# Kernel tuning notes

Hardware: AMD Instinct MI355X
Metric: run time of the kernel (lower is better)

## Reference

```python
import jax, jax.numpy as jnp
import numpy as np

B, N, F, G, H = 8, 1024, 512, 128, 8
D = F // H  # head_dim = 64


def setup_inputs() -> dict:
    key = jax.random.key(0)
    ks = jax.random.split(key, 24)
    def lin(k, fan_in, shape):
        return jax.random.normal(k, shape, jnp.float32) / np.sqrt(fan_in)
    return {
        "features": jax.random.normal(ks[0], (B, N, F), jnp.float32),
        "geometry": jax.random.normal(ks[1], (B, N, G), jnp.float32),
        "coords": jax.random.normal(ks[2], (B, N, 3), jnp.float32),
        # nnx.MultiHeadAttention params (q/k/v/out dense, with bias)
        "wq": lin(ks[3], F, (F, F)), "bq": jnp.zeros((F,), jnp.float32),
        "wk": lin(ks[4], F, (F, F)), "bk": jnp.zeros((F,), jnp.float32),
        "wv": lin(ks[5], F, (F, F)), "bv": jnp.zeros((F,), jnp.float32),
        "wo": lin(ks[6], F, (F, F)), "bo": jnp.zeros((F,), jnp.float32),
        # geometry q/k/v linears
        "gq_w": lin(ks[7], G, (G, F)), "gq_b": jnp.zeros((F,), jnp.float32),
        "gk_w": lin(ks[8], G, (G, F)), "gk_b": jnp.zeros((F,), jnp.float32),
        "gv_w": lin(ks[9], G, (G, F)), "gv_b": jnp.zeros((F,), jnp.float32),
        # distance MLP: Linear(1->H), gelu, Linear(H->H)
        "d1_w": lin(ks[10], 1, (1, H)), "d1_b": jnp.zeros((H,), jnp.float32),
        "d2_w": lin(ks[11], H, (H, H)), "d2_b": jnp.zeros((H,), jnp.float32),
        # output projection
        "op_w": lin(ks[12], F, (F, F)), "op_b": jnp.zeros((F,), jnp.float32),
    }


def _forward(features, geometry, coords,
             wq, bq, wk, bk, wv, bv, wo, bo,
             gq_w, gq_b, gk_w, gk_b, gv_w, gv_b,
             d1_w, d1_b, d2_w, d2_b, op_w, op_b):
    scale = jnp.sqrt(jnp.float32(D))
    # --- standard multi-head self-attention branch (nnx.MultiHeadAttention) ---
    q = (features @ wq + bq).reshape(B, N, H, D)
    k = (features @ wk + bk).reshape(B, N, H, D)
    v = (features @ wv + bv).reshape(B, N, H, D)
    scores = jnp.einsum("bqhd,bkhd->bhqk", q, k) / scale
    attn = jax.nn.softmax(scores, axis=-1)
    feat_att = jnp.einsum("bhqk,bkhd->bqhd", attn, v).reshape(B, N, F)
    feat_att = feat_att @ wo + bo
    # --- geometry attention branch ---
    gq = geometry @ gq_w + gq_b
    gk = geometry @ gk_w + gk_b
    gv = geometry @ gv_w + gv_b
    g_scores = jnp.einsum("bqd,bkd->bqk", gq, gk) / scale
    # pairwise distances (B,N,N,1); clamp for sqrt-at-zero safety (diagonal)
    diff = coords[:, :, None, :] - coords[:, None, :, :]
    dist = jnp.sqrt(jnp.maximum(jnp.sum(diff * diff, -1, keepdims=True), 1e-12))
    dw = jax.nn.gelu(dist @ d1_w + d1_b) @ d2_w + d2_b  # (B,N,N,H)
    # transpose to (B,H,N,N) then mean over heads == mean over last axis
    g_scores = g_scores + jnp.mean(dw, axis=-1)
    g_attn = jax.nn.softmax(g_scores, axis=-1)
    geom_att = jnp.einsum("bqk,bkd->bqd", g_attn, gv)
    return (feat_att + geom_att) @ op_w + op_b


def reference(features, geometry, coords,
              wq, bq, wk, bk, wv, bv, wo, bo,
              gq_w, gq_b, gk_w, gk_b, gv_w, gv_b,
              d1_w, d1_b, d2_w, d2_b, op_w, op_b):
    return _forward(features, geometry, coords,
                    wq, bq, wk, bk, wv, bv, wo, bo,
                    gq_w, gq_b, gk_w, gk_b, gv_w, gv_b,
                    d1_w, d1_b, d2_w, d2_b, op_w, op_b)
```

## Files before the change

### kernel.cpp

```cpp
#include <hip/hip_runtime.h>

typedef __bf16 bf16_t;
typedef __bf16 bf16x8 __attribute__((ext_vector_type(8)));
typedef __bf16 bf16x4v __attribute__((ext_vector_type(4)));
typedef float f32x4 __attribute__((ext_vector_type(4)));

#define MFMA16(a, b, c) __builtin_amdgcn_mfma_f32_16x16x32_bf16((a), (b), (c), 0, 0, 0)

static constexpr int B_ = 8, N_ = 1024, F_ = 512, H_ = 8;
static constexpr int M_ = B_ * N_;
static constexpr float LOG2E = 1.4426950408889634f;

__device__ __forceinline__ void gl_lds16(const bf16_t* gsrc, bf16_t* ldst) {
  __builtin_amdgcn_global_load_lds(
      (const __attribute__((address_space(1))) void*)gsrc,
      (__attribute__((address_space(3))) void*)ldst, 16, 0, 0);
}

__device__ __forceinline__ float gelu_tanh(float u) {
  float g = 0.7978845608028654f * fmaf(0.044715f * u * u, u, u);
  float e = __expf(2.f * g);
  float t = 1.f - 2.f / (e + 1.f);
  return 0.5f * u * (1.f + t);
}

struct PrepArgs {
  const float *features, *geometry;
  const float *wq, *wk, *wv, *wo, *op_w;
  const float *gq_w, *gk_w, *gv_w;
  const float *bq, *bk, *bv, *gq_b, *gv_b;
  const float *d1w, *d1b, *d2w, *d2b;
  bf16_t *featBF, *geomBF, *WqkvT, *GqvT2, *WoT, *OpT;
  float *bqkv, *gqvb2, *dlut;
};

static constexpr int PR_C0 = 4096;
static constexpr int PR_C1 = PR_C0 + 1024;
static constexpr int PR_WQ = PR_C1 + 256;
static constexpr int PR_WK = PR_WQ + 256;
static constexpr int PR_WV = PR_WK + 256;
static constexpr int PR_WO = PR_WV + 256;
static constexpr int PR_OP = PR_WO + 256;
static constexpr int PR_GVT = PR_OP + 64;
static constexpr int PR_WEFF = PR_GVT + 4;
static constexpr int PR_BEFF = PR_WEFF + 1;
static constexpr int PR_B1 = PR_BEFF + 6;
static constexpr int PR_B2 = PR_B1 + 2;
static constexpr int PR_LUT = PR_B2 + 16;
static constexpr int PR_TOTAL = PR_LUT;

__device__ __forceinline__ void prep_cast(const float* __restrict__ in,
                                          bf16_t* __restrict__ out, int blk) {
  int i = blk * 256 + threadIdx.x;
  float4 v = ((const float4*)in)[i];
  bf16x4v o;
  o[0] = (bf16_t)v.x; o[1] = (bf16_t)v.y; o[2] = (bf16_t)v.z; o[3] = (bf16_t)v.w;
  ((bf16x4v*)out)[i] = o;
}

__device__ __forceinline__ void prep_transpose(const float* __restrict__ W,
                                               bf16_t* __restrict__ Wt,
                                               int K, int N, int ldo, int idx,
                                               float (*t)[33]) {
  const int bx = idx & 15, by = idx >> 4;
  const int kb = by * 32, cb = bx * 32;
  const int tx = threadIdx.x & 31, ty = threadIdx.x >> 5;
#pragma unroll
  for (int i = 0; i < 4; ++i)
    t[ty * 4 + i][tx] = W[(long)(kb + ty * 4 + i) * N + cb + tx];
  __syncthreads();
#pragma unroll
  for (int i = 0; i < 4; ++i)
    Wt[(long)(cb + ty * 4 + i) * ldo + kb + tx] = (bf16_t)t[tx][ty * 4 + i];
}

__device__ __forceinline__ bf16x8 cvt2x4(float4 a, float4 b) {
  bf16x8 v;
  v[0] = (bf16_t)a.x; v[1] = (bf16_t)a.y; v[2] = (bf16_t)a.z; v[3] = (bf16_t)a.w;
  v[4] = (bf16_t)b.x; v[5] = (bf16_t)b.y; v[6] = (bf16_t)b.z; v[7] = (bf16_t)b.w;
  return v;
}

__global__ __launch_bounds__(256) void k_prep(PrepArgs p) {
  __shared__ alignas(16) char psh[16384];
  float (*tsh)[33] = (float (*)[33])psh;
  const int blk = blockIdx.x;
  if (blk < PR_C0) {
    prep_cast(p.features, p.featBF, blk);
  } else if (blk < PR_C1) {
    prep_cast(p.geometry, p.geomBF, blk - PR_C0);
  } else if (blk < PR_WQ) {
    prep_transpose(p.wq, p.WqkvT, 512, 512, 512, blk - PR_C1, tsh);
  } else if (blk < PR_WK) {
    prep_transpose(p.wk, p.WqkvT + 512 * 512, 512, 512, 512, blk - PR_WQ, tsh);
  } else if (blk < PR_WV) {
    prep_transpose(p.wv, p.WqkvT + 1024 * 512, 512, 512, 512, blk - PR_WK, tsh);
  } else if (blk < PR_WO) {
    prep_transpose(p.wo, p.WoT, 512, 512, 512, blk - PR_WV, tsh);
  } else if (blk < PR_OP) {
    prep_transpose(p.op_w, p.OpT, 512, 512, 512, blk - PR_WO, tsh);
  } else if (blk < PR_GVT) {
    prep_transpose(p.gv_w, p.GqvT2 + 128 * 128, 128, 512, 128, blk - PR_OP, tsh);
  } else if (blk < PR_WEFF) {
    bf16_t (*As)[64] = (bf16_t (*)[64])psh;
    bf16_t (*Bs)[64] = (bf16_t (*)[64])(psh + 8192);
    const int wb = blk - PR_GVT;
    const int gBrow = (wb >> 1) * 64;
    const int hBcol = (wb & 1) * 64;
    const int tid = threadIdx.x;
    const int w4 = tid >> 6, lane = tid & 63;
    const int lr = lane & 15, lg = lane >> 4;
    const int wr = w4 >> 1, wc = w4 & 1;
    const int srow = tid >> 2, scol = (tid & 3) << 4;
    f32x4 zero = {0.f, 0.f, 0.f, 0.f};
    f32x4 acc[2][2] = {{zero, zero}, {zero, zero}};
    for (int f0 = 0; f0 < 512; f0 += 64) {
#pragma unroll
      for (int hh = 0; hh < 2; ++hh) {
        const long offA = (long)(gBrow + srow) * 512 + f0 + scol + hh * 8;
        float4 a0 = *(const float4*)(p.gk_w + offA);
        float4 a1 = *(const float4*)(p.gk_w + offA + 4);
        *(bf16x8*)(&As[srow][scol + hh * 8]) = cvt2x4(a0, a1);
        const long offB = (long)(hBcol + srow) * 512 + f0 + scol + hh * 8;
        float4 b0 = *(const float4*)(p.gq_w + offB);
        float4 b1 = *(const float4*)(p.gq_w + offB + 4);
        *(bf16x8*)(&Bs[srow][scol + hh * 8]) = cvt2x4(b0, b1);
      }
      __syncthreads();
#pragma unroll
      for (int ks = 0; ks < 2; ++ks) {
        bf16x8 a[2], b[2];
#pragma unroll
        for (int i = 0; i < 2; ++i) {
          a[i] = *(const bf16x8*)(&As[wr * 32 + i * 16 + lr][ks * 32 + lg * 8]);
          b[i] = *(const bf16x8*)(&Bs[wc * 32 + i * 16 + lr][ks * 32 + lg * 8]);
        }
#pragma unroll
        for (int mf = 0; mf < 2; ++mf)
#pragma unroll
          for (int nf = 0; nf < 2; ++nf)
            acc[mf][nf] = MFMA16(a[mf], b[nf], acc[mf][nf]);
      }
      __syncthreads();
    }
#pragma unroll
    for (int mf = 0; mf < 2; ++mf)
#pragma unroll
      for (int nf = 0; nf < 2; ++nf)
#pragma unroll
        for (int rg = 0; rg < 4; ++rg) {
          const int row = gBrow + wr * 32 + mf * 16 + lg * 4 + rg;
          const int col = hBcol + wc * 32 + nf * 16 + lr;
          p.GqvT2[(long)row * 128 + col] = (bf16_t)acc[mf][nf][rg];
        }
  } else if (blk < PR_BEFF) {
    const int g = threadIdx.x;
    if (g < 128) {
      float s = 0.f;
      for (int f = 0; f < 512; ++f) s = fmaf(p.gq_b[f], p.gk_w[(long)g * 512 + f], s);
      p.gqvb2[g] = s;
    }
  } else if (blk < PR_B1) {
    int i = (blk - PR_BEFF) * 256 + threadIdx.x;
    p.bqkv[i] = i < 512 ? p.bq[i] : (i < 1024 ? p.bk[i - 512] : p.bv[i - 1024]);
  } else if (blk < PR_B2) {
    int i = (blk - PR_B1) * 256 + threadIdx.x;
    p.gqvb2[128 + i] = p.gv_b[i];
  } else {
    int i = (blk - PR_B2) * 256 + threadIdx.x;
    float d = (i + 0.5f) * (16.f / 4096.f);
    float s = 0.f;
#pragma unroll
    for (int h = 0; h < 8; ++h) s += p.d2b[h];
    s *= 0.125f;
#pragma unroll
    for (int j = 0; j < 8; ++j) {
      float w2 = 0.f;
#pragma unroll
      for (int h = 0; h < 8; ++h) w2 += p.d2w[j * 8 + h];
      s = fmaf(gelu_tanh(fmaf(d, p.d1w[j], p.d1b[j])), w2 * 0.125f, s);
    }
    p.dlut[i] = s;
  }
}

struct GemmArgs {
  const bf16_t* A; const bf16_t* Bt;
  const float* bias; const float* addSrc; const bf16_t* addSrcB;
  const float* coords; const float* lut;
  float* outF; bf16_t* outB;
  bf16_t* outT;
  int vtileFrom;
  long strideAb; long strideBb;
  int lda, ldb, K, ldout;
  float scale;
};

__device__ __forceinline__ void gemm128_core(const GemmArgs& g, int mBase, int cBase,
                                             bf16_t (*As)[64], bf16_t (*Bs)[64]) {
  const int tid = threadIdx.x;
  const int w = tid >> 6, lane = tid & 63;
  const int lr = lane & 15, lg = lane >> 4;
  const int wr = w >> 1, wc = w & 1;
  const int batch = mBase >> 10;

  const int srow = lane >> 3;
  const int scol = (lane & 7) * 8;
  const bf16_t* Ag = g.A + (long)batch * g.strideAb +
                     (long)((mBase & 1023) + w * 32 + srow) * g.lda + scol;
  const bf16_t* Bg = g.Bt + (long)batch * g.strideBb +
                     (long)(cBase + w * 32 + srow) * g.ldb + scol;
  bf16_t* Al = &As[w * 32][0];
  bf16_t* Bl = &Bs[w * 32][0];

  f32x4 zero = {0.f, 0.f, 0.f, 0.f};
  f32x4 acc[4][4];
#pragma unroll
  for (int i = 0; i < 4; ++i)
#pragma unroll
    for (int j = 0; j < 4; ++j) acc[i][j] = zero;

  for (int k0 = 0; k0 < g.K; k0 += 64) {
#pragma unroll
    for (int is = 0; is < 4; ++is) {
      gl_lds16(Ag + (long)(is * 8) * g.lda + k0, Al + is * 8 * 64);
      gl_lds16(Bg + (long)(is * 8) * g.ldb + k0, Bl + is * 8 * 64);
    }
    __syncthreads();
#pragma unroll
    for (int ks = 0; ks < 2; ++ks) {
      bf16x8 a[4], b[4];
#pragma unroll
      for (int i = 0; i < 4; ++i) {
        a[i] = *(const bf16x8*)(&As[wr * 64 + i * 16 + lr][ks * 32 + lg * 8]);
        b[i] = *(const bf16x8*)(&Bs[wc * 64 + i * 16 + lr][ks * 32 + lg * 8]);
      }
#pragma unroll
      for (int mf = 0; mf < 4; ++mf)
#pragma unroll
        for (int nf = 0; nf < 4; ++nf)
          acc[mf][nf] = MFMA16(a[mf], b[nf], acc[mf][nf]);
    }
    __syncthreads();
  }

  const int c0 = cBase + wc * 64;
  float bias4[4];
#pragma unroll
  for (int nf = 0; nf < 4; ++nf)
    bias4[nf] = g.bias ? g.bias[c0 + nf * 16 + lr] : 0.f;
  const bool vtile = (g.outT != nullptr) && (cBase >= g.vtileFrom);
#pragma unroll
  for (int mf = 0; mf < 4; ++mf) {
    const int r0 = mBase + wr * 64 + mf * 16 + lg * 4;
    const int r0b = r0 & 1023;
#pragma unroll
    for (int nf = 0; nf < 4; ++nf) {
      const int c = c0 + nf * 16 + lr;
      if (vtile) {
        bf16x4v vv;
#pragma unroll
        for (int rg = 0; rg < 4; ++rg)
          vv[rg] = (bf16_t)(acc[mf][nf][rg] * g.scale + bias4[nf]);
        *(bf16x4v*)(&g.outT[((long)batch * 512 + (c - g.vtileFrom)) * 1024 + r0b]) = vv;
      } else {
#pragma unroll
        for (int rg = 0; rg < 4; ++rg) {
          const int r = r0 + rg;
          float v = acc[mf][nf][rg] * g.scale + bias4[nf];
          if (g.addSrc) v += g.addSrc[(long)r * g.ldout + c];
          const long oi = (long)r * g.ldout + c;
          if (g.outF) g.outF[oi] = v;
          if (g.outB) g.outB[oi] = (bf16_t)v;
        }
      }
    }
  }
}

__global__ __launch_bounds__(256) void k_gemm128_dual(GemmArgs g1, GemmArgs g2) {
  __shared__ alignas(16) bf16_t As[128][64];
  __shared__ alignas(16) bf16_t Bs[128][64];
  const int bx = blockIdx.x;
  if (bx < 768) {
    gemm128_core(g1, (bx / 12) * 128, (bx % 12) * 128, As, Bs);
  } else {
    const int i = bx - 768;
    gemm128_core(g2, (i / 5) * 128, (i % 5) * 128, As, Bs);
  }
}

__device__ __forceinline__ void gemm128_dist(const GemmArgs& g, int mBase, int cBase,
                                             char* smemc) {
  bf16_t (*As)[64] = (bf16_t (*)[64])smemc;
  bf16_t (*Bs)[64] = (bf16_t (*)[64])(smemc + 16384);
  bf16_t* Lut = (bf16_t*)(smemc + 32768);
  const int tid = threadIdx.x;
  const int w = tid >> 6, lane = tid & 63;
  const int lr = lane & 15, lg = lane >> 4;
  const int wr = w >> 1, wc = w & 1;
  const int batch = mBase >> 10;

  {
    const float4* src = (const float4*)g.lut;
#pragma unroll
    for (int i = 0; i < 4; ++i) {
      float4 v = src[tid + i * 256];
      bf16x4v o;
      o[0] = (bf16_t)(v.x * LOG2E); o[1] = (bf16_t)(v.y * LOG2E);
      o[2] = (bf16_t)(v.z * LOG2E); o[3] = (bf16_t)(v.w * LOG2E);
      ((bf16x4v*)Lut)[tid + i * 256] = o;
    }
  }

  const int srow = lane >> 3;
  const int scol = (lane & 7) * 8;
  const bf16_t* Ag = g.A + (long)batch * g.strideAb +
                     (long)((mBase & 1023) + w * 32 + srow) * g.lda + scol;
  const bf16_t* Bg = g.Bt + (long)batch * g.strideBb +
                     (long)(cBase + w * 32 + srow) * g.ldb + scol;
  bf16_t* Al = &As[w * 32][0];
  bf16_t* Bl = &Bs[w * 32][0];

  f32x4 zero = {0.f, 0.f, 0.f, 0.f};
  f32x4 acc[4][4];
#pragma unroll
  for (int i = 0; i < 4; ++i)
#pragma unroll
    for (int j = 0; j < 4; ++j) acc[i][j] = zero;

  for (int k0 = 0; k0 < g.K; k0 += 64) {
#pragma unroll
    for (int is = 0; is < 4; ++is) {
      gl_lds16(Ag + (long)(is * 8) * g.lda + k0, Al + is * 8 * 64);
      gl_lds16(Bg + (long)(is * 8) * g.ldb + k0, Bl + is * 8 * 64);
    }
    __syncthreads();
#pragma unroll
    for (int ks = 0; ks < 2; ++ks) {
      bf16x8 a[4], b[4];
#pragma unroll
      for (int i = 0; i < 4; ++i) {
        a[i] = *(const bf16x8*)(&As[wr * 64 + i * 16 + lr][ks * 32 + lg * 8]);
        b[i] = *(const bf16x8*)(&Bs[wc * 64 + i * 16 + lr][ks * 32 + lg * 8]);
      }
#pragma unroll
      for (int mf = 0; mf < 4; ++mf)
#pragma unroll
        for (int nf = 0; nf < 4; ++nf)
          acc[mf][nf] = MFMA16(a[mf], b[nf], acc[mf][nf]);
    }
    __syncthreads();
  }

  const int c0 = cBase + wc * 64;
  float ckx[4], cky[4], ckz[4];
#pragma unroll
  for (int nf = 0; nf < 4; ++nf) {
    const float* ck = g.coords + ((long)batch * 1024 + c0 + nf * 16 + lr) * 3;
    ckx[nf] = ck[0]; cky[nf] = ck[1]; ckz[nf] = ck[2];
  }
#pragma unroll
  for (int mf = 0; mf < 4; ++mf) {
    const int r0 = mBase + wr * 64 + mf * 16 + lg * 4;
    float cqx[4], cqy[4], cqz[4];
#pragma unroll
    for (int rg = 0; rg < 4; ++rg) {
      const float* cq = g.coords + ((long)batch * 1024 + ((r0 + rg) & 1023)) * 3;
      cqx[rg] = cq[0]; cqy[rg] = cq[1]; cqz[rg] = cq[2];
    }
#pragma unroll
    for (int nf = 0; nf < 4; ++nf) {
      const int c = c0 + nf * 16 + lr;
#pragma unroll
      for (int rg = 0; rg < 4; ++rg) {
        const int r = r0 + rg;
        float v = acc[mf][nf][rg] * g.scale;
        float dx = cqx[rg] - ckx[nf], dy = cqy[rg] - cky[nf], dz = cqz[rg] - ckz[nf];
        float d = sqrtf(fmaxf(dx * dx + dy * dy + dz * dz, 1e-12f));
        int idx = (int)(d * 256.f);
        idx = idx > 4095 ? 4095 : idx;
        g.outB[(long)r * g.ldout + c] = (bf16_t)exp2f(v + (float)Lut[idx]);
      }
    }
  }
}

__device__ __forceinline__ void flash_core(const bf16_t* __restrict__ QKV,
                                           const bf16_t* __restrict__ Vt,
                                           bf16_t* __restrict__ fatt,
                                           int qx, int bh, char* smemc) {
  bf16_t (*Ks)[64][64] = (bf16_t (*)[64][64])smemc;
  bf16_t (*Vs)[64][64] = (bf16_t (*)[64][64])(smemc + 16384);
  char* Plb = smemc + 32768;
  const int wave = threadIdx.x >> 6, lane = threadIdx.x & 63;
  const int lr = lane & 15, lg = (lane >> 4) & 3;
  const int b = bh >> 3, h = bh & 7;
  const int qbase = qx * 128 + wave * 32;

  const bf16_t* Qb = QKV + (long)b * 1024 * 1536 + h * 64;
  const bf16_t* Kb = Qb + 512;
  const bf16_t* Vg = Vt + ((long)b * 512 + h * 64) * 1024;

  constexpr float SCL = 0.18033688011112042f;
  bf16x8 q_[2][2];
#pragma unroll
  for (int qf = 0; qf < 2; ++qf)
#pragma unroll
    for (int dh = 0; dh < 2; ++dh) {
      bf16x8 raw = *(const bf16x8*)(Qb + (long)(qbase + qf * 16 + lr) * 1536 +
                                    dh * 32 + lg * 8);
#pragma unroll
      for (int j = 0; j < 8; ++j) q_[qf][dh][j] = (bf16_t)((float)raw[j] * SCL);
    }
  bf16x8 onesb;
#pragma unroll
  for (int j = 0; j < 8; ++j) onesb[j] = (bf16_t)1.0f;

  const int srow = lane >> 3;
  const int scol = (((lane & 7) ^ srow) << 3);
  const bf16_t* KgB = Kb + (long)(wave * 16 + srow) * 1536 + scol;
  const bf16_t* VgB = Vg + (long)(wave * 16 + srow) * 1024 + scol;

  auto stage = [&](int buf, int kt) {
#pragma unroll
    for (int i = 0; i < 2; ++i) {
      gl_lds16(KgB + (long)(kt + i * 8) * 1536, &Ks[buf][wave * 16 + i * 8][0]);
      gl_lds16(VgB + (long)(i * 8) * 1024 + kt, &Vs[buf][wave * 16 + i * 8][0]);
    }
  };

  f32x4 zero = {0.f, 0.f, 0.f, 0.f};
  f32x4 oacc[2][4] = {{zero, zero, zero, zero}, {zero, zero, zero, zero}};
  f32x4 oL[2] = {zero, zero};
  const int swz = (lr & 7) << 4;
  const int swp = (lr & 6) << 3;
  char* PlW = Plb + wave * 2048;

  stage(0, 0);
  asm volatile("s_waitcnt vmcnt(0)" ::: "memory");
  __syncthreads();

  auto tile = [&](const int buf, int t) __attribute__((always_inline)) {
    if (t < 15) stage(buf ^ 1, (t + 1) * 64);
    const char* KB = (const char*)&Ks[buf][0][0];
    const char* VB = (const char*)&Vs[buf][0][0];
#pragma unroll
    for (int kk = 0; kk < 2; ++kk) {
      f32x4 S[2][2];
      __builtin_amdgcn_s_setprio(1);
#pragma unroll
      for (int kh = 0; kh < 2; ++kh) {
        const int row = kk * 32 + kh * 16 + lr;
        bf16x8 k0 = *(const bf16x8*)(KB + row * 128 + ((lg * 16) ^ swz));
        bf16x8 k1 = *(const bf16x8*)(KB + row * 128 + ((64 + lg * 16) ^ swz));
#pragma unroll
        for (int qf = 0; qf < 2; ++qf) {
          f32x4 tt = MFMA16(k0, q_[qf][0], zero);
          S[qf][kh] = MFMA16(k1, q_[qf][1], tt);
        }
      }
      __builtin_amdgcn_s_setprio(0);
#pragma unroll
      for (int qf = 0; qf < 2; ++qf)
#pragma unroll
        for (int kh = 0; kh < 2; ++kh) {
          bf16x4v pp;
#pragma unroll
          for (int r = 0; r < 4; ++r) pp[r] = (bf16_t)exp2f(S[qf][kh][r]);
          *(bf16x4v*)(PlW + qf * 1024 + lr * 64 + ((kh * 32 + lg * 8) ^ swp)) = pp;
        }
      asm volatile("s_waitcnt lgkmcnt(0)" ::: "memory");
      const bf16x8 pa0 = *(const bf16x8*)(PlW + lr * 64 + ((lg * 16) ^ swp));
      const bf16x8 pa1 = *(const bf16x8*)(PlW + 1024 + lr * 64 + ((lg * 16) ^ swp));
      __builtin_amdgcn_s_setprio(1);
#pragma unroll
      for (int ct = 0; ct < 4; ++ct) {
        const int vrow = ct * 16 + lr;
        bf16x8 vf = *(const bf16x8*)(VB + vrow * 128 + ((kk * 64 + lg * 16) ^ swz));
        oacc[0][ct] = MFMA16(pa0, vf, oacc[0][ct]);
        oacc[1][ct] = MFMA16(pa1, vf, oacc[1][ct]);
      }
      oL[0] = MFMA16(pa0, onesb, oL[0]);
      oL[1] = MFMA16(pa1, onesb, oL[1]);
      __builtin_amdgcn_s_setprio(0);
    }
    asm volatile("s_waitcnt vmcnt(0)" ::: "memory");
    __syncthreads();
  };

  for (int tt = 0; tt < 8; ++tt) {
    tile(0, tt * 2);
    tile(1, tt * 2 + 1);
  }

#pragma unroll
  for (int qf = 0; qf < 2; ++qf)
#pragma unroll
    for (int r = 0; r < 4; ++r) {
      float inv = 1.f / oL[qf][r];
      int q = qbase + qf * 16 + lg * 4 + r;
      bf16_t* orow = fatt + ((long)b * 1024 + q) * 512 + h * 64;
#pragma unroll
      for (int ct = 0; ct < 4; ++ct)
        orow[ct * 16 + lr] = (bf16_t)(oacc[qf][ct][r] * inv);
    }
}

__global__ __launch_bounds__(256) void k_gsc_flash(GemmArgs g,
                                                   const bf16_t* __restrict__ QKV,
                                                   const bf16_t* __restrict__ Vt,
                                                   bf16_t* __restrict__ fatt) {
  __shared__ alignas(16) char smem[40960];
  const int bx = blockIdx.x;
  if (bx < 512) {
    gemm128_dist(g, (bx >> 3) * 128, (bx & 7) * 128, smem);
  } else {
    const int fid = bx - 512;
    flash_core(QKV, Vt, fatt, fid & 7, fid >> 3, smem);
  }
}

template <int RSUM>
__device__ __forceinline__ void m64_loop(const GemmArgs& g, int mBase, int cBase,
                                         bf16_t (*As)[64], bf16_t (*Bs)[64],
                                         f32x4 (*acc)[2], f32x4* lacc) {
  const int tid = threadIdx.x;
  const int w = tid >> 6, lane = tid & 63;
  const int lr = lane & 15, lg = lane >> 4;
  const int wr = w >> 1, wc = w & 1;
  const int batch = mBase >> 10;

  const int srow = lane >> 3;
  const int scol = (lane & 7) * 8;
  const bf16_t* Ag = g.A + (long)batch * g.strideAb +
                     (long)((mBase & 1023) + w * 16 + srow) * g.lda + scol;
  const bf16_t* Bg = g.Bt + (long)batch * g.strideBb +
                     (long)(cBase + w * 16 + srow) * g.ldb + scol;
  bf16_t* Al = &As[w * 16][0];
  bf16_t* Bl = &Bs[w * 16][0];

  bf16x8 onesb;
#pragma unroll
  for (int j = 0; j < 8; ++j) onesb[j] = (bf16_t)1.0f;

  for (int k0 = 0; k0 < g.K; k0 += 64) {
#pragma unroll
    for (int is = 0; is < 2; ++is) {
      gl_lds16(Ag + (long)(is * 8) * g.lda + k0, Al + is * 8 * 64);
      gl_lds16(Bg + (long)(is * 8) * g.ldb + k0, Bl + is * 8 * 64);
    }
    __syncthreads();
#pragma unroll
    for (int ks = 0; ks < 2; ++ks) {
      bf16x8 a[2], b[2];
#pragma unroll
      for (int i = 0; i < 2; ++i) {
        a[i] = *(const bf16x8*)(&As[wr * 32 + i * 16 + lr][ks * 32 + lg * 8]);
        b[i] = *(const bf16x8*)(&Bs[wc * 32 + i * 16 + lr][ks * 32 + lg * 8]);
      }
#pragma unroll
      for (int mf = 0; mf < 2; ++mf)
#pragma unroll
        for (int nf = 0; nf < 2; ++nf)
          acc[mf][nf] = MFMA16(a[mf], b[nf], acc[mf][nf]);
      if constexpr (RSUM) {
#pragma unroll
        for (int mf = 0; mf < 2; ++mf)
          lacc[mf] = MFMA16(a[mf], onesb, lacc[mf]);
      }
    }
    __syncthreads();
  }
}

__global__ __launch_bounds__(256) void k_gemm_m64(GemmArgs g) {
  __shared__ alignas(16) bf16_t As[64][64];
  __shared__ alignas(16) bf16_t Bs[64][64];
  const int tid = threadIdx.x;
  const int w = tid >> 6, lane = tid & 63;
  const int lr = lane & 15, lg = lane >> 4;
  const int wr = w >> 1, wc = w & 1;
  const int mBase = blockIdx.y * 64, cBase = blockIdx.x * 64;

  f32x4 zero = {0.f, 0.f, 0.f, 0.f};
  f32x4 acc[2][2] = {{zero, zero}, {zero, zero}};
  m64_loop<0>(g, mBase, cBase, As, Bs, acc, nullptr);

  const int c0 = cBase + wc * 32;
  float bias2[2];
#pragma unroll
  for (int nf = 0; nf < 2; ++nf)
    bias2[nf] = g.bias ? g.bias[c0 + nf * 16 + lr] : 0.f;
#pragma unroll
  for (int mf = 0; mf < 2; ++mf) {
    const int r0 = mBase + wr * 32 + mf * 16 + lg * 4;
#pragma unroll
    for (int nf = 0; nf < 2; ++nf) {
      const int c = c0 + nf * 16 + lr;
#pragma unroll
      for (int rg = 0; rg < 4; ++rg) {
        const int r = r0 + rg;
        float v = acc[mf][nf][rg] * g.scale + bias2[nf];
        const long oi = (long)r * g.ldout + c;
        if (g.outF) g.outF[oi] = v;
        if (g.outB) g.outB[oi] = (bf16_t)v;
      }
    }
  }
}

__global__ __launch_bounds__(256) void k_comb(GemmArgs gF, GemmArgs gG,
                                              bf16_t* __restrict__ outB) {
  __shared__ alignas(16) bf16_t As[64][64];
  __shared__ alignas(16) bf16_t Bs[64][64];
  const int tid = threadIdx.x;
  const int w = tid >> 6, lane = tid & 63;
  const int lr = lane & 15, lg = lane >> 4;
  const int wr = w >> 1, wc = w & 1;
  const int mBase = blockIdx.y * 64, cBase = blockIdx.x * 64;

  f32x4 zero = {0.f, 0.f, 0.f, 0.f};
  f32x4 acc1[2][2] = {{zero, zero}, {zero, zero}};
  f32x4 acc2[2][2] = {{zero, zero}, {zero, zero}};
  f32x4 lacc[2] = {zero, zero};
  m64_loop<0>(gF, mBase, cBase, As, Bs, acc1, nullptr);
  m64_loop<1>(gG, mBase, cBase, As, Bs, acc2, lacc);

  const int c0 = cBase + wc * 32;
  float bias2[2];
#pragma unroll
  for (int nf = 0; nf < 2; ++nf)
    bias2[nf] = gF.bias[c0 + nf * 16 + lr];
#pragma unroll
  for (int mf = 0; mf < 2; ++mf) {
    const int r0 = mBase + wr * 32 + mf * 16 + lg * 4;
    float linv[4];
#pragma unroll
    for (int rg = 0; rg < 4; ++rg) linv[rg] = 1.f / lacc[mf][rg];
#pragma unroll
    for (int nf = 0; nf < 2; ++nf) {
      const int c = c0 + nf * 16 + lr;
#pragma unroll
      for (int rg = 0; rg < 4; ++rg) {
        const int r = r0 + rg;
        float v = acc2[mf][nf][rg] * linv[rg] + acc1[mf][nf][rg] + bias2[nf];
        outB[(long)r * 512 + c] = (bf16_t)v;
      }
    }
  }
}

extern "C" void kernel_launch(void* const* d_in, const int* in_sizes, int n_in,
                              void* d_out, int out_size, void* d_ws, size_t ws_size,
                              hipStream_t stream) {
  const float* features = (const float*)d_in[0];
  const float* geometry = (const float*)d_in[1];
  const float* coords   = (const float*)d_in[2];
  const float* wq = (const float*)d_in[3];  const float* bq = (const float*)d_in[4];
  const float* wk = (const float*)d_in[5];  const float* bk = (const float*)d_in[6];
  const float* wv = (const float*)d_in[7];  const float* bv = (const float*)d_in[8];
  const float* wo = (const float*)d_in[9];  const float* bo = (const float*)d_in[10];
  const float* gq_w = (const float*)d_in[11]; const float* gq_b = (const float*)d_in[12];
  const float* gk_w = (const float*)d_in[13]; const float* gk_b = (const float*)d_in[14];
  const float* gv_w = (const float*)d_in[15]; const float* gv_b = (const float*)d_in[16];
  const float* d1_w = (const float*)d_in[17]; const float* d1_b = (const float*)d_in[18];
  const float* d2_w = (const float*)d_in[19]; const float* d2_b = (const float*)d_in[20];
  const float* op_w = (const float*)d_in[21]; const float* op_b = (const float*)d_in[22];
  (void)gk_b;

  size_t off = 0;
  auto carve = [&](size_t bytes) {
    void* p = (char*)d_ws + off;
    off += (bytes + 255) & ~(size_t)255;
    return p;
  };
  bf16_t* featBF = (bf16_t*)carve((size_t)M_ * F_ * 2);
  bf16_t* geomBF = (bf16_t*)carve((size_t)M_ * 128 * 2);
  bf16_t* WqkvT  = (bf16_t*)carve((size_t)1536 * 512 * 2);
  bf16_t* GqvT2  = (bf16_t*)carve((size_t)640 * 128 * 2);
  bf16_t* WoT    = (bf16_t*)carve((size_t)512 * 512 * 2);
  bf16_t* OpT    = (bf16_t*)carve((size_t)512 * 512 * 2);
  float*  bqkv   = (float*)carve(1536 * 4);
  float*  gqvb2  = (float*)carve(640 * 4);
  float*  dlut   = (float*)carve(4096 * 4);
  bf16_t* QKV    = (bf16_t*)carve((size_t)M_ * 1536 * 2);
  bf16_t* GQeff  = (bf16_t*)carve((size_t)M_ * 128 * 2);
  bf16_t* Vt     = (bf16_t*)carve((size_t)B_ * 512 * 1024 * 2);
  bf16_t* GVt    = (bf16_t*)carve((size_t)B_ * 512 * 1024 * 2);
  bf16_t* Pun    = (bf16_t*)carve((size_t)M_ * 1024 * 2);
  bf16_t* fatt   = (bf16_t*)carve((size_t)M_ * 512 * 2);
  bf16_t* combB  = (bf16_t*)carve((size_t)M_ * 512 * 2);
  if (off > ws_size) return;

  PrepArgs p;
  p.features = features; p.geometry = geometry;
  p.wq = wq; p.wk = wk; p.wv = wv; p.wo = wo; p.op_w = op_w;
  p.gq_w = gq_w; p.gk_w = gk_w; p.gv_w = gv_w;
  p.bq = bq; p.bk = bk; p.bv = bv; p.gq_b = gq_b; p.gv_b = gv_b;
  p.d1w = d1_w; p.d1b = d1_b; p.d2w = d2_w; p.d2b = d2_b;
  p.featBF = featBF; p.geomBF = geomBF; p.WqkvT = WqkvT; p.GqvT2 = GqvT2;
  p.WoT = WoT; p.OpT = OpT;
  p.bqkv = bqkv; p.gqvb2 = gqvb2; p.dlut = dlut;
  k_prep<<<PR_TOTAL, 256, 0, stream>>>(p);

  auto mk = [](const bf16_t* A, long sAb, int lda, const bf16_t* Bt, long sBb, int ldb,
               int K, const float* bias, const float* addSrc, const bf16_t* addSrcB,
               float* outF, bf16_t* outB, int ldout, float scale,
               const float* coords, const float* lut, bf16_t* outT, int vtileFrom) {
    GemmArgs g;
    g.A = A; g.Bt = Bt; g.bias = bias; g.addSrc = addSrc; g.addSrcB = addSrcB;
    g.coords = coords; g.lut = lut; g.outF = outF; g.outB = outB; g.outT = outT;
    g.vtileFrom = vtileFrom;
    g.strideAb = sAb; g.strideBb = sBb; g.lda = lda; g.ldb = ldb;
    g.K = K; g.ldout = ldout; g.scale = scale;
    return g;
  };

  k_gemm128_dual<<<1088, 256, 0, stream>>>(
      mk(featBF, (long)1024 * 512, 512, WqkvT, 0, 512, 512,
         bqkv, nullptr, nullptr, nullptr, QKV, 1536, 1.f, nullptr, nullptr, Vt, 1024),
      mk(geomBF, (long)1024 * 128, 128, GqvT2, 0, 128, 128,
         gqvb2, nullptr, nullptr, nullptr, GQeff, 128, 1.f, nullptr, nullptr, GVt, 128));
  k_gsc_flash<<<1024, 256, 0, stream>>>(
      mk(GQeff, (long)1024 * 128, 128, geomBF, (long)1024 * 128, 128, 128,
         nullptr, nullptr, nullptr, nullptr, Pun, 1024, 0.125f * LOG2E,
         coords, dlut, nullptr, 1 << 30),
      QKV, Vt, fatt);
  k_comb<<<dim3(8, 128), 256, 0, stream>>>(
      mk(fatt, (long)1024 * 512, 512, WoT, 0, 512, 512,
         bo, nullptr, nullptr, nullptr, nullptr, 512, 1.f, nullptr, nullptr,
         nullptr, 1 << 30),
      mk(Pun, (long)1024 * 1024, 1024, GVt, (long)512 * 1024, 1024, 1024,
         nullptr, nullptr, nullptr, nullptr, nullptr, 512, 1.f, nullptr, nullptr,
         nullptr, 1 << 30),
      combB);
  k_gemm_m64<<<dim3(8, 128), 256, 0, stream>>>(
      mk(combB, (long)1024 * 512, 512, OpT, 0, 512, 512,
         op_b, nullptr, nullptr, (float*)d_out, nullptr, 512, 1.f, nullptr, nullptr,
         nullptr, 1 << 30));
}
```

Baseline: 160.3 us.

## Triple-buffer K/V staging in flash attention with one barrier per tile

Replaces the double-buffered K/V LDS pipeline in the flash-attention path with a three-buffer rotation. Loads run two tiles ahead, and each iteration waits with vmcnt(4) and a single barrier instead of a full vmcnt(0) plus syncthreads at the end of every tile. The goal is to hide global-to-LDS latency behind more compute. In exchange, LDS for the fused kernel grows from 40KB to 56KB, which may cut the number of resident blocks per CU, and the extra space is also allocated for the GEMM blocks that share this kernel.

Result: slower. 164.7 us (+2.7%).

```diff
diff --git a/kernel.cpp b/kernel.cpp
--- a/kernel.cpp
+++ b/kernel.cpp
@@ -390,9 +390,7 @@
                                            const bf16_t* __restrict__ Vt,
                                            bf16_t* __restrict__ fatt,
                                            int qx, int bh, char* smemc) {
-  bf16_t (*Ks)[64][64] = (bf16_t (*)[64][64])smemc;
-  bf16_t (*Vs)[64][64] = (bf16_t (*)[64][64])(smemc + 16384);
-  char* Plb = smemc + 32768;
+  char* Plb = smemc + 49152;
   const int wave = threadIdx.x >> 6, lane = threadIdx.x & 63;
   const int lr = lane & 15, lg = (lane >> 4) & 3;
   const int b = bh >> 3, h = bh & 7;
@@ -422,11 +420,13 @@
   const bf16_t* KgB = Kb + (long)(wave * 16 + srow) * 1536 + scol;
   const bf16_t* VgB = Vg + (long)(wave * 16 + srow) * 1024 + scol;
 
-  auto stage = [&](int buf, int kt) {
+  auto stage = [&](char* buf, int kt) {
+    bf16_t* Kd = (bf16_t*)buf;
+    bf16_t* Vd = (bf16_t*)(buf + 8192);
 #pragma unroll
     for (int i = 0; i < 2; ++i) {
-      gl_lds16(KgB + (long)(kt + i * 8) * 1536, &Ks[buf][wave * 16 + i * 8][0]);
-      gl_lds16(VgB + (long)(i * 8) * 1024 + kt, &Vs[buf][wave * 16 + i * 8][0]);
+      gl_lds16(KgB + (long)(kt + i * 8) * 1536, Kd + (wave * 16 + i * 8) * 64);
+      gl_lds16(VgB + (long)(i * 8) * 1024 + kt, Vd + (wave * 16 + i * 8) * 64);
     }
   };
 
@@ -437,14 +437,13 @@
   const int swp = (lr & 6) << 3;
   char* PlW = Plb + wave * 2048;
 
-  stage(0, 0);
-  asm volatile("s_waitcnt vmcnt(0)" ::: "memory");
-  __syncthreads();
-
-  auto tile = [&](const int buf, int t) __attribute__((always_inline)) {
-    if (t < 15) stage(buf ^ 1, (t + 1) * 64);
-    const char* KB = (const char*)&Ks[buf][0][0];
-    const char* VB = (const char*)&Vs[buf][0][0];
+  char* p0 = smemc;
+  char* p1 = smemc + 16384;
+  char* p2 = smemc + 32768;
+  stage(p0, 0);
+  stage(p1, 64);
+
+  auto compute = [&](const char* KB, const char* VB) __attribute__((always_inline)) {
 #pragma unroll
     for (int kk = 0; kk < 2; ++kk) {
       f32x4 S[2][2];
@@ -471,6 +470,7 @@
           *(bf16x4v*)(PlW + qf * 1024 + lr * 64 + ((kh * 32 + lg * 8) ^ swp)) = pp;
         }
       asm volatile("s_waitcnt lgkmcnt(0)" ::: "memory");
+      __builtin_amdgcn_sched_barrier(0);
       const bf16x8 pa0 = *(const bf16x8*)(PlW + lr * 64 + ((lg * 16) ^ swp));
       const bf16x8 pa1 = *(const bf16x8*)(PlW + 1024 + lr * 64 + ((lg * 16) ^ swp));
       __builtin_amdgcn_s_setprio(1);
@@ -485,14 +485,20 @@
       oL[1] = MFMA16(pa1, onesb, oL[1]);
       __builtin_amdgcn_s_setprio(0);
     }
-    asm volatile("s_waitcnt vmcnt(0)" ::: "memory");
-    __syncthreads();
   };
 
-  for (int tt = 0; tt < 8; ++tt) {
-    tile(0, tt * 2);
-    tile(1, tt * 2 + 1);
-  }
+  for (int t = 0; t < 15; ++t) {
+    asm volatile("s_waitcnt vmcnt(4)" ::: "memory");
+    __builtin_amdgcn_s_barrier();
+    asm volatile("" ::: "memory");
+    if (t + 2 < 16) stage(p2, (t + 2) * 64);
+    compute(p0, p0 + 8192);
+    char* tmp = p0; p0 = p1; p1 = p2; p2 = tmp;
+  }
+  asm volatile("s_waitcnt vmcnt(0)" ::: "memory");
+  __builtin_amdgcn_s_barrier();
+  asm volatile("" ::: "memory");
+  compute(p0, p0 + 8192);
 
 #pragma unroll
   for (int qf = 0; qf < 2; ++qf)
@@ -511,7 +517,7 @@
                                                    const bf16_t* __restrict__ QKV,
                                                    const bf16_t* __restrict__ Vt,
                                                    bf16_t* __restrict__ fatt) {
-  __shared__ alignas(16) char smem[40960];
+  __shared__ alignas(16) char smem[57344];
   const int bx = blockIdx.x;
   if (bx < 512) {
     gemm128_dist(g, (bx >> 3) * 128, (bx & 7) * 128, smem);
```
